# Kernel tuning notes

Hardware: AMD Instinct MI355X
Metric: run time of the kernel (lower is better)

## Reference

```python
import jax, jax.numpy as jnp
import numpy as np

N_NODES = 100000
N_EDGES = 640000
EMB = 128
BATCH = 16384
N_REL = 2
HIDDEN = [128, 64, 32]
LN_EPS = 1e-5
NORM_EPS = 1e-12


def setup_inputs() -> dict:
    key = jax.random.key(0)
    ks = jax.random.split(key, 24)
    inp = {}
    inp["user_indices"] = jax.random.randint(ks[0], (BATCH,), 0, N_NODES)
    inp["item_indices"] = jax.random.randint(ks[1], (BATCH,), 0, N_NODES)
    inp["edge_index"] = jax.random.randint(ks[2], (2, N_EDGES), 0, N_NODES)
    inp["edge_type"] = jax.random.randint(ks[3], (N_EDGES,), 0, N_REL)
    inp["edge_weight"] = jax.random.uniform(ks[4], (N_EDGES,), dtype=jnp.float32)
    # parameters
    s = 1.0 / np.sqrt(EMB)
    inp["embedding"] = jax.random.normal(ks[5], (N_NODES, EMB), jnp.float32) * 0.02
    inp["w1_rel"] = jax.random.normal(ks[6], (N_REL, EMB, EMB), jnp.float32) * s
    inp["w1_root"] = jax.random.normal(ks[7], (EMB, EMB), jnp.float32) * s
    inp["b1"] = jnp.zeros((EMB,), jnp.float32)
    inp["ln_g"] = jnp.ones((EMB,), jnp.float32)
    inp["ln_b"] = jnp.zeros((EMB,), jnp.float32)
    inp["w2_rel"] = jax.random.normal(ks[8], (N_REL, EMB, EMB), jnp.float32) * s
    inp["w2_root"] = jax.random.normal(ks[9], (EMB, EMB), jnp.float32) * s
    inp["b2"] = jnp.zeros((EMB,), jnp.float32)
    dims = [2 * EMB] + HIDDEN
    for i in range(len(HIDDEN)):
        inp[f"mlp_w{i}"] = jax.random.normal(ks[10 + i], (dims[i], dims[i + 1]), jnp.float32) / np.sqrt(dims[i])
        inp[f"mlp_b{i}"] = jnp.zeros((dims[i + 1],), jnp.float32)
    d_out = HIDDEN[-1] + EMB
    inp["out_w"] = jax.random.normal(ks[20], (d_out, 1), jnp.float32) / np.sqrt(d_out)
    inp["out_b"] = jnp.zeros((1,), jnp.float32)
    return inp


def rgcn_layer(x, edge_index, edge_type, edge_weight, w_rel, w_root, bias):
    # x: [N, D]; edge_index: [2, E]; per-relation linear on gathered source feats,
    # weighted scatter-add into destination nodes, plus root transform + bias.
    src, dst = edge_index[0], edge_index[1]
    x_j = x[src]  # [E, D] gather
    msg = jnp.zeros((x_j.shape[0], w_rel.shape[2]), x.dtype)
    for r in range(w_rel.shape[0]):  # small fixed relation count
        msg = msg + jnp.where((edge_type == r)[:, None], x_j @ w_rel[r], 0.0)
    msg = msg * edge_weight[:, None]
    agg = jax.ops.segment_sum(msg, dst, num_segments=x.shape[0])
    return agg + x @ w_root + bias


def layer_norm(x, g, b):
    mu = jnp.mean(x, axis=-1, keepdims=True)
    var = jnp.mean(jnp.square(x - mu), axis=-1, keepdims=True)
    return (x - mu) * jax.lax.rsqrt(var + LN_EPS) * g + b


def l2_normalize(x):
    n = jnp.sqrt(jnp.sum(jnp.square(x), axis=-1, keepdims=True))
    return x / jnp.maximum(n, NORM_EPS)


def reference(user_indices, item_indices, edge_index, edge_type, edge_weight,
              embedding, w1_rel, w1_root, b1, ln_g, ln_b, w2_rel, w2_root, b2,
              mlp_w0, mlp_b0, mlp_w1, mlp_b1, mlp_w2, mlp_b2, out_w, out_b):
    x = embedding  # embedding(arange(N)) == full table
    x = rgcn_layer(x, edge_index, edge_type, edge_weight, w1_rel, w1_root, b1)
    x = jax.nn.relu(x)
    # dropout is identity in eval mode
    x = layer_norm(x, ln_g, ln_b)
    x = rgcn_layer(x, edge_index, edge_type, edge_weight, w2_rel, w2_root, b2)

    u = x[user_indices]  # [B, D]
    v = x[item_indices]
    gmf = l2_normalize(u) * l2_normalize(v)  # [B, D]
    h = jnp.concatenate([u, v], axis=-1)  # [B, 2D]
    for w, b in ((mlp_w0, mlp_b0), (mlp_w1, mlp_b1), (mlp_w2, mlp_b2)):
        h = jax.nn.relu(h @ w + b)
    final = jnp.concatenate([gmf, h], axis=-1)  # [B, D + 32]
    score = jax.nn.sigmoid(final @ out_w + out_b)
    return jnp.squeeze(score, axis=-1)
```

## Files before the change

### kernel.cpp

```cpp
#include <hip/hip_runtime.h>
#include <cstddef>
#include <cstdint>

#define N_NODES 100000
#define N_EDGES 640000
#define EMBD    128
#define NBATCH  16384
#define CHUNK   1024
#define NCHUNK  ((N_NODES + CHUNK - 1) / CHUNK)

typedef short bf16x8 __attribute__((ext_vector_type(8)));
typedef float f32x4  __attribute__((ext_vector_type(4)));

__device__ __forceinline__ unsigned pack_split(float x) {
    unsigned u  = __float_as_uint(x);
    unsigned hi = (u + 0x7fffu + ((u >> 16) & 1u)) & 0xffff0000u;
    float    lo = x - __uint_as_float(hi);
    unsigned ul = __float_as_uint(lo);
    unsigned lw = ((ul + 0x7fffu + ((ul >> 16) & 1u)) >> 16) & 0xffffu;
    return hi | lw;
}
__device__ __forceinline__ float unpack_split(unsigned u) {
    return __uint_as_float(u & 0xffff0000u) + __uint_as_float(u << 16);
}

__global__ __launch_bounds__(256) void pack_kernel(
    const float* __restrict__ in, unsigned* __restrict__ out, int n)
{
    const int i = blockIdx.x * 256 + threadIdx.x;
    if (i < n) out[i] = pack_split(in[i]);
}

__global__ __launch_bounds__(256) void hist_kernel(
    const int* __restrict__ ei, int* __restrict__ cursor, int E)
{
    const int e = blockIdx.x * 256 + threadIdx.x;
    if (e < E) atomicAdd(&cursor[ei[E + e]], 1);
}

__global__ __launch_bounds__(256) void scan_local(
    int* __restrict__ cursor, int* __restrict__ bsum, int n)
{
    __shared__ int part[256];
    const int t    = threadIdx.x;
    const int base = blockIdx.x * CHUNK + t * 4;
    int v[4];
    int s = 0;
#pragma unroll
    for (int i = 0; i < 4; ++i) {
        const int idx = base + i;
        v[i] = (idx < n) ? cursor[idx] : 0;
        s += v[i];
    }
    part[t] = s;
    __syncthreads();
    for (int off = 1; off < 256; off <<= 1) {
        const int add = (t >= off) ? part[t - off] : 0;
        __syncthreads();
        part[t] += add;
        __syncthreads();
    }
    if (t == 255) bsum[blockIdx.x] = part[255];
    int run = (t == 0) ? 0 : part[t - 1];
#pragma unroll
    for (int i = 0; i < 4; ++i) {
        const int idx = base + i;
        if (idx < n) { cursor[idx] = run; run += v[i]; }
    }
}

__global__ __launch_bounds__(128) void scan_bsum(int* __restrict__ bsum)
{
    __shared__ int part[128];
    const int t = threadIdx.x;
    const int v = (t < NCHUNK) ? bsum[t] : 0;
    part[t] = v;
    __syncthreads();
    for (int off = 1; off < 128; off <<= 1) {
        const int add = (t >= off) ? part[t - off] : 0;
        __syncthreads();
        part[t] += add;
        __syncthreads();
    }
    if (t < NCHUNK) bsum[t] = part[t] - v;
}

__global__ __launch_bounds__(256) void scan_add(
    int* __restrict__ cursor, const int* __restrict__ bsum, int n)
{
    const int off  = bsum[blockIdx.x];
    const int base = blockIdx.x * CHUNK + threadIdx.x * 4;
#pragma unroll
    for (int i = 0; i < 4; ++i) {
        const int idx = base + i;
        if (idx < n) cursor[idx] += off;
    }
}

__global__ __launch_bounds__(256) void bucket_kernel(
    const int* __restrict__ ei, const int* __restrict__ et,
    const float* __restrict__ ew, int* __restrict__ cursor,
    int2* __restrict__ srec, int E)
{
    const int e = blockIdx.x * 256 + threadIdx.x;
    if (e >= E) return;
    const int src = ei[e];
    const int dst = ei[E + e];
    const int r   = et[e];
    const int pos = atomicAdd(&cursor[dst], 1);
    srec[pos] = make_int2(src | (r << 17), __float_as_int(ew[e]));
}

__global__ __launch_bounds__(256) void accum_csr(
    const unsigned* __restrict__ xp, const int2* __restrict__ srec,
    const int* __restrict__ cursor, unsigned* __restrict__ Ap, int N)
{
    const int wid  = blockIdx.x * 4 + (threadIdx.x >> 6);
    const int lane = threadIdx.x & 63;
    const int s = (wid == 0) ? 0 : cursor[wid - 1];
    const int e = cursor[wid];

    float ax = 0.f, ay = 0.f, bx = 0.f, by = 0.f;
    int i = s;
    for (; i + 3 < e; i += 4) {
        const int2 r0 = srec[i];
        const int2 r1 = srec[i + 1];
        const int2 r2 = srec[i + 2];
        const int2 r3 = srec[i + 3];
        const uint2 g0 = ((const uint2*)(xp + (size_t)(r0.x & 0x1FFFF) * EMBD))[lane];
        const uint2 g1 = ((const uint2*)(xp + (size_t)(r1.x & 0x1FFFF) * EMBD))[lane];
        const uint2 g2 = ((const uint2*)(xp + (size_t)(r2.x & 0x1FFFF) * EMBD))[lane];
        const uint2 g3 = ((const uint2*)(xp + (size_t)(r3.x & 0x1FFFF) * EMBD))[lane];
        const float w0 = __int_as_float(r0.y);
        const float w1 = __int_as_float(r1.y);
        const float w2 = __int_as_float(r2.y);
        const float w3 = __int_as_float(r3.y);
        {
            const float vx = unpack_split(g0.x), vy = unpack_split(g0.y);
            if (r0.x & (1 << 17)) { bx += vx * w0; by += vy * w0; }
            else                  { ax += vx * w0; ay += vy * w0; }
        }
        {
            const float vx = unpack_split(g1.x), vy = unpack_split(g1.y);
            if (r1.x & (1 << 17)) { bx += vx * w1; by += vy * w1; }
            else                  { ax += vx * w1; ay += vy * w1; }
        }
        {
            const float vx = unpack_split(g2.x), vy = unpack_split(g2.y);
            if (r2.x & (1 << 17)) { bx += vx * w2; by += vy * w2; }
            else                  { ax += vx * w2; ay += vy * w2; }
        }
        {
            const float vx = unpack_split(g3.x), vy = unpack_split(g3.y);
            if (r3.x & (1 << 17)) { bx += vx * w3; by += vy * w3; }
            else                  { ax += vx * w3; ay += vy * w3; }
        }
    }
    for (; i < e; ++i) {
        const int2 r0 = srec[i];
        const uint2 g0 = ((const uint2*)(xp + (size_t)(r0.x & 0x1FFFF) * EMBD))[lane];
        const float w0 = __int_as_float(r0.y);
        const float vx = unpack_split(g0.x), vy = unpack_split(g0.y);
        if (r0.x & (1 << 17)) { bx += vx * w0; by += vy * w0; }
        else                  { ax += vx * w0; ay += vy * w0; }
    }
    ((uint2*)(Ap + (size_t)wid * EMBD))[lane]             = make_uint2(pack_split(ax), pack_split(ay));
    ((uint2*)(Ap + ((size_t)N + wid) * EMBD))[lane]       = make_uint2(pack_split(bx), pack_split(by));
}

__global__ __launch_bounds__(256) void gemm_mfma(
    const unsigned* __restrict__ S0, const unsigned* __restrict__ S1,
    const unsigned* __restrict__ S2,
    const float* __restrict__ wrel, const float* __restrict__ wroot,
    const float* __restrict__ bias, const float* __restrict__ lng,
    const float* __restrict__ lnb, void* __restrict__ outv,
    int M, int do_ln)
{
    __shared__ unsigned short AsH[128 * 40], AsL[128 * 40];
    __shared__ unsigned short BsH[128 * 40], BsL[128 * 40];
    __shared__ float lnbuf[2][128][2];

    const int t    = threadIdx.x;
    const int wave = t >> 6;
    const int lane = t & 63;
    const int q    = lane >> 4;
    const int n    = lane & 15;
    const int wrow = wave & 1;
    const int wcol = wave >> 1;
    const int m0   = blockIdx.x * 128;

    const int arow  = t >> 1;
    const int ahalf = t & 1;
    const int bcol  = t & 127;
    const int bkh   = t >> 7;

    f32x4 acc[4][4];
#pragma unroll
    for (int rt = 0; rt < 4; ++rt)
#pragma unroll
        for (int ct = 0; ct < 4; ++ct)
            acc[rt][ct] = (f32x4){0.f, 0.f, 0.f, 0.f};

    for (int kc = 0; kc < 12; ++kc) {
        const unsigned* Sp  = (kc < 4) ? S0 : (kc < 8) ? S1 : S2;
        const int koff      = (kc & 3) * 32;
        const float* Wsrc   = (kc < 8) ? (wrel + (size_t)kc * 32 * EMBD)
                                       : (wroot + (size_t)(kc - 8) * 32 * EMBD);

        __syncthreads();

        {
            const int rg = m0 + arow;
            uint4 u[4];
            if (rg < M) {
                const unsigned* p = Sp + (size_t)rg * EMBD + koff + ahalf * 16;
                u[0] = *(const uint4*)(p);
                u[1] = *(const uint4*)(p + 4);
                u[2] = *(const uint4*)(p + 8);
                u[3] = *(const uint4*)(p + 12);
            } else {
                u[0] = u[1] = u[2] = u[3] = make_uint4(0u, 0u, 0u, 0u);
            }
            unsigned* dh = (unsigned*)AsH + arow * 20 + ahalf * 8;
            unsigned* dl = (unsigned*)AsL + arow * 20 + ahalf * 8;
            const unsigned* uu = (const unsigned*)u;
#pragma unroll
            for (int i = 0; i < 8; ++i) {
                const unsigned e0 = uu[2 * i], e1 = uu[2 * i + 1];
                dh[i] = (e1 & 0xffff0000u) | (e0 >> 16);
                dl[i] = (e1 << 16) | (e0 & 0xffffu);
            }
        }
        {
            unsigned p[16];
#pragma unroll
            for (int j = 0; j < 16; ++j)
                p[j] = pack_split(Wsrc[(size_t)(bkh * 16 + j) * EMBD + bcol]);
            unsigned* dh = (unsigned*)BsH + bcol * 20 + bkh * 8;
            unsigned* dl = (unsigned*)BsL + bcol * 20 + bkh * 8;
#pragma unroll
            for (int i = 0; i < 8; ++i) {
                const unsigned e0 = p[2 * i], e1 = p[2 * i + 1];
                dh[i] = (e1 & 0xffff0000u) | (e0 >> 16);
                dl[i] = (e1 << 16) | (e0 & 0xffffu);
            }
        }
        __syncthreads();

        bf16x8 ah[4], al[4], bh[4], bl[4];
#pragma unroll
        for (int rt = 0; rt < 4; ++rt) {
            const int r = wrow * 64 + rt * 16 + n;
            ah[rt] = *(const bf16x8*)&AsH[r * 40 + q * 8];
            al[rt] = *(const bf16x8*)&AsL[r * 40 + q * 8];
        }
#pragma unroll
        for (int ct = 0; ct < 4; ++ct) {
            const int c = wcol * 64 + ct * 16 + n;
            bh[ct] = *(const bf16x8*)&BsH[c * 40 + q * 8];
            bl[ct] = *(const bf16x8*)&BsL[c * 40 + q * 8];
        }
#pragma unroll
        for (int rt = 0; rt < 4; ++rt)
#pragma unroll
            for (int ct = 0; ct < 4; ++ct) {
                acc[rt][ct] = __builtin_amdgcn_mfma_f32_16x16x32_bf16(ah[rt], bh[ct], acc[rt][ct], 0, 0, 0);
                acc[rt][ct] = __builtin_amdgcn_mfma_f32_16x16x32_bf16(ah[rt], bl[ct], acc[rt][ct], 0, 0, 0);
                acc[rt][ct] = __builtin_amdgcn_mfma_f32_16x16x32_bf16(al[rt], bh[ct], acc[rt][ct], 0, 0, 0);
            }
    }

    float bb[4], gg[4], tb[4];
#pragma unroll
    for (int ct = 0; ct < 4; ++ct) {
        const int c = wcol * 64 + ct * 16 + n;
        bb[ct] = bias[c];
        gg[ct] = do_ln ? lng[c] : 0.f;
        tb[ct] = do_ln ? lnb[c] : 0.f;
    }

    if (do_ln) {
#pragma unroll
        for (int rt = 0; rt < 4; ++rt)
#pragma unroll
            for (int r = 0; r < 4; ++r) {
                float s = 0.f, sq = 0.f;
#pragma unroll
                for (int ct = 0; ct < 4; ++ct) {
                    float v = acc[rt][ct][r] + bb[ct];
                    v = fmaxf(v, 0.f);
                    acc[rt][ct][r] = v;
                    s += v; sq += v * v;
                }
#pragma unroll
                for (int off = 1; off < 16; off <<= 1) {
                    s  += __shfl_xor(s,  off, 64);
                    sq += __shfl_xor(sq, off, 64);
                }
                if (n == 0) {
                    const int row = wrow * 64 + rt * 16 + q * 4 + r;
                    lnbuf[wcol][row][0] = s;
                    lnbuf[wcol][row][1] = sq;
                }
            }
        __syncthreads();
        unsigned* outp = (unsigned*)outv;
#pragma unroll
        for (int rt = 0; rt < 4; ++rt)
#pragma unroll
            for (int r = 0; r < 4; ++r) {
                const int row = wrow * 64 + rt * 16 + q * 4 + r;
                const int rg  = m0 + row;
                const float s    = lnbuf[0][row][0] + lnbuf[1][row][0];
                const float sq   = lnbuf[0][row][1] + lnbuf[1][row][1];
                const float mu   = s * (1.0f / 128.0f);
                const float var  = sq * (1.0f / 128.0f) - mu * mu;
                const float rstd = rsqrtf(var + 1e-5f);
                if (rg < M) {
#pragma unroll
                    for (int ct = 0; ct < 4; ++ct) {
                        const int c = wcol * 64 + ct * 16 + n;
                        const float v = (acc[rt][ct][r] - mu) * rstd * gg[ct] + tb[ct];
                        outp[(size_t)rg * EMBD + c] = pack_split(v);
                    }
                }
            }
    } else {
        float* outp = (float*)outv;
#pragma unroll
        for (int rt = 0; rt < 4; ++rt)
#pragma unroll
            for (int r = 0; r < 4; ++r) {
                const int rg = m0 + wrow * 64 + rt * 16 + q * 4 + r;
                if (rg < M) {
#pragma unroll
                    for (int ct = 0; ct < 4; ++ct) {
                        const int c = wcol * 64 + ct * 16 + n;
                        outp[(size_t)rg * EMBD + c] = acc[rt][ct][r] + bb[ct];
                    }
                }
            }
    }
}

__global__ __launch_bounds__(256) void head_kernel(
    const float* __restrict__ x2, const int* __restrict__ ui, const int* __restrict__ vi,
    const float* __restrict__ mw0, const float* __restrict__ mb0,
    const float* __restrict__ mw1, const float* __restrict__ mb1,
    const float* __restrict__ mw2, const float* __restrict__ mb2,
    const float* __restrict__ ow, const float* __restrict__ ob,
    float* __restrict__ out, int B)
{
    __shared__ float h0[16][256];
    __shared__ float h1[16][128];
    __shared__ float h2[16][64];
    __shared__ float h3[16][32];
    __shared__ float ps_u[16][16], ps_v[16][16];
    __shared__ float inv_nunv[16];
    __shared__ float pg[16][16], ph[16][16];

    const int t   = threadIdx.x;
    const int bb0 = blockIdx.x * 16;

    for (int r = 0; r < 16; ++r) {
        const int b   = bb0 + r;
        const int idx = (t < 128) ? ui[b] : vi[b];
        const int c   = t & 127;
        h0[r][t] = x2[(size_t)idx * EMBD + c];
    }
    __syncthreads();

    {
        const int row = t >> 4, sub = t & 15;
        float su = 0.f, sv = 0.f;
#pragma unroll
        for (int k = 0; k < 8; ++k) {
            const float a = h0[row][sub + 16 * k];       su += a * a;
            const float b = h0[row][128 + sub + 16 * k]; sv += b * b;
        }
        ps_u[row][sub] = su; ps_v[row][sub] = sv;
    }
    __syncthreads();
    if (t < 16) {
        float su = 0.f, sv = 0.f;
#pragma unroll
        for (int k = 0; k < 16; ++k) { su += ps_u[t][k]; sv += ps_v[t][k]; }
        const float nu = fmaxf(sqrtf(su), 1e-12f);
        const float nv = fmaxf(sqrtf(sv), 1e-12f);
        inv_nunv[t] = 1.0f / (nu * nv);
    }
    __syncthreads();

    {
        const int c = t & 127, rr = t >> 7;
        float acc[8];
#pragma unroll
        for (int j = 0; j < 8; ++j) acc[j] = 0.f;
        for (int i = 0; i < 256; i += 4) {
            const float w0 = mw0[(i + 0) * 128 + c];
            const float w1 = mw0[(i + 1) * 128 + c];
            const float w2 = mw0[(i + 2) * 128 + c];
            const float w3 = mw0[(i + 3) * 128 + c];
#pragma unroll
            for (int j = 0; j < 8; ++j) {
                const float4 a = *(const float4*)&h0[rr * 8 + j][i];
                acc[j] += a.x * w0 + a.y * w1 + a.z * w2 + a.w * w3;
            }
        }
        const float bv = mb0[c];
#pragma unroll
        for (int j = 0; j < 8; ++j) h1[rr * 8 + j][c] = fmaxf(acc[j] + bv, 0.f);
    }
    __syncthreads();

    {
        const int c = t & 63, g = t >> 6;
        float acc[4] = {0.f, 0.f, 0.f, 0.f};
        for (int i = 0; i < 128; i += 4) {
            const float w0 = mw1[(i + 0) * 64 + c];
            const float w1 = mw1[(i + 1) * 64 + c];
            const float w2 = mw1[(i + 2) * 64 + c];
            const float w3 = mw1[(i + 3) * 64 + c];
#pragma unroll
            for (int j = 0; j < 4; ++j) {
                const float4 a = *(const float4*)&h1[g * 4 + j][i];
                acc[j] += a.x * w0 + a.y * w1 + a.z * w2 + a.w * w3;
            }
        }
        const float bv = mb1[c];
#pragma unroll
        for (int j = 0; j < 4; ++j) h2[g * 4 + j][c] = fmaxf(acc[j] + bv, 0.f);
    }
    __syncthreads();

    {
        const int c = t & 31, g = t >> 5;
        float acc[2] = {0.f, 0.f};
        for (int i = 0; i < 64; i += 4) {
            const float w0 = mw2[(i + 0) * 32 + c];
            const float w1 = mw2[(i + 1) * 32 + c];
            const float w2 = mw2[(i + 2) * 32 + c];
            const float w3 = mw2[(i + 3) * 32 + c];
#pragma unroll
            for (int j = 0; j < 2; ++j) {
                const float4 a = *(const float4*)&h2[g * 2 + j][i];
                acc[j] += a.x * w0 + a.y * w1 + a.z * w2 + a.w * w3;
            }
        }
        const float bv = mb2[c];
#pragma unroll
        for (int j = 0; j < 2; ++j) h3[g * 2 + j][c] = fmaxf(acc[j] + bv, 0.f);
    }
    __syncthreads();

    {
        const int row = t >> 4, sub = t & 15;
        float pgv = 0.f;
#pragma unroll
        for (int k = 0; k < 8; ++k) {
            const int c = sub + 16 * k;
            pgv += h0[row][c] * h0[row][128 + c] * ow[c];
        }
        const float phv = h3[row][sub]      * ow[128 + sub]
                        + h3[row][sub + 16] * ow[144 + sub];
        pg[row][sub] = pgv; ph[row][sub] = phv;
    }
    __syncthreads();
    if (t < 16) {
        float sg = 0.f, sh = 0.f;
#pragma unroll
        for (int k = 0; k < 16; ++k) { sg += pg[t][k]; sh += ph[t][k]; }
        const float z = sg * inv_nunv[t] + sh + ob[0];
        out[bb0 + t] = 1.0f / (1.0f + expf(-z));
    }
}

extern "C" void kernel_launch(void* const* d_in, const int* in_sizes, int n_in,
                              void* d_out, int out_size, void* d_ws, size_t ws_size,
                              hipStream_t stream)
{
    const int*   ui      = (const int*)d_in[0];
    const int*   vi      = (const int*)d_in[1];
    const int*   ei      = (const int*)d_in[2];
    const int*   et      = (const int*)d_in[3];
    const float* ew      = (const float*)d_in[4];
    const float* emb     = (const float*)d_in[5];
    const float* w1_rel  = (const float*)d_in[6];
    const float* w1_root = (const float*)d_in[7];
    const float* b1      = (const float*)d_in[8];
    const float* ln_g    = (const float*)d_in[9];
    const float* ln_b    = (const float*)d_in[10];
    const float* w2_rel  = (const float*)d_in[11];
    const float* w2_root = (const float*)d_in[12];
    const float* b2      = (const float*)d_in[13];
    const float* mw0     = (const float*)d_in[14];
    const float* mb0     = (const float*)d_in[15];
    const float* mw1     = (const float*)d_in[16];
    const float* mb1     = (const float*)d_in[17];
    const float* mw2     = (const float*)d_in[18];
    const float* mb2     = (const float*)d_in[19];
    const float* ow      = (const float*)d_in[20];
    const float* ob      = (const float*)d_in[21];
    float* out = (float*)d_out;

    const int N = N_NODES, E = N_EDGES, B = NBATCH;

    unsigned* Ap    = (unsigned*)d_ws;
    unsigned* xslot = Ap + (size_t)2 * N * EMBD;
    int2*     srec   = (int2*)(xslot + (size_t)N * EMBD);
    int*      cursor = (int*)(srec + E);
    int*      bsum   = cursor + N;

    float* x2 = (float*)Ap;

    pack_kernel<<<(N * EMBD + 255) / 256, 256, 0, stream>>>(emb, xslot, N * EMBD);

    hipMemsetAsync(cursor, 0, N * sizeof(int), stream);
    hist_kernel<<<(E + 255) / 256, 256, 0, stream>>>(ei, cursor, E);
    scan_local<<<NCHUNK, 256, 0, stream>>>(cursor, bsum, N);
    scan_bsum<<<1, 128, 0, stream>>>(bsum);
    scan_add<<<NCHUNK, 256, 0, stream>>>(cursor, bsum, N);
    bucket_kernel<<<(E + 255) / 256, 256, 0, stream>>>(ei, et, ew, cursor, srec, E);

    accum_csr<<<N / 4, 256, 0, stream>>>(xslot, srec, cursor, Ap, N);
    gemm_mfma<<<(N + 127) / 128, 256, 0, stream>>>(
        Ap, Ap + (size_t)N * EMBD, xslot,
        w1_rel, w1_root, b1, ln_g, ln_b,
        (void*)xslot , N, 1);

    accum_csr<<<N / 4, 256, 0, stream>>>(xslot, srec, cursor, Ap, N);
    gemm_mfma<<<(N + 127) / 128, 256, 0, stream>>>(
        Ap, Ap + (size_t)N * EMBD, xslot,
        w2_rel, w2_root, b2, nullptr, nullptr,
        (void*)x2 , N, 0);

    head_kernel<<<B / 16, 256, 0, stream>>>(
        x2, ui, vi, mw0, mb0, mw1, mb1, mw2, mb2, ow, ob, out, B);
}
```

Baseline: 501.2 us.

## Pre-pack GEMM weights once and register-prefetch the next K chunk

A new kernel converts both layers' relation and root weights once into transposed bf16 hi/lo planes. Each GEMM block now loads those planes with vector loads instead of re-splitting strided fp32 weights for every tile. The GEMM main loop prefetches the next K chunk into registers while MFMAs run on the current chunk, writes LDS with vector stores and adds a 3-block occupancy hint. The embedding pack and edge histogram kernels are fused into one launch. The fallback path for a small workspace indexes a packing array past its 8 entries, and the extra live prefetch registers may limit occupancy.

Result: slower. 535.4 us (+6.8%).

```diff
diff --git a/kernel.cpp b/kernel.cpp
--- a/kernel.cpp
+++ b/kernel.cpp
@@ -24,18 +24,38 @@
     return __uint_as_float(u & 0xffff0000u) + __uint_as_float(u << 16);
 }
 
-__global__ __launch_bounds__(256) void pack_kernel(
-    const float* __restrict__ in, unsigned* __restrict__ out, int n)
+__global__ __launch_bounds__(256) void pack_hist(
+    const float* __restrict__ emb, unsigned* __restrict__ xslot,
+    const int* __restrict__ ei, int* __restrict__ cursor, int n, int E)
 {
     const int i = blockIdx.x * 256 + threadIdx.x;
-    if (i < n) out[i] = pack_split(in[i]);
-}
-
-__global__ __launch_bounds__(256) void hist_kernel(
-    const int* __restrict__ ei, int* __restrict__ cursor, int E)
-{
-    const int e = blockIdx.x * 256 + threadIdx.x;
-    if (e < E) atomicAdd(&cursor[ei[E + e]], 1);
+    if (i < n) xslot[i] = pack_split(emb[i]);
+    if (i < E) atomicAdd(&cursor[ei[E + i]], 1);
+}
+
+__global__ void wpack_kernel(
+    const float* __restrict__ w1_rel, const float* __restrict__ w1_root,
+    const float* __restrict__ w2_rel, const float* __restrict__ w2_root,
+    unsigned short* __restrict__ WtH1, unsigned short* __restrict__ WtL1,
+    unsigned short* __restrict__ WtH2, unsigned short* __restrict__ WtL2)
+{
+    const int col = blockIdx.x;
+    const int k   = threadIdx.x;
+    const size_t o = (size_t)col * 384 + k;
+    {
+        const float x = (k < 256) ? w1_rel[(size_t)k * EMBD + col]
+                                  : w1_root[(size_t)(k - 256) * EMBD + col];
+        const unsigned p = pack_split(x);
+        WtH1[o] = (unsigned short)(p >> 16);
+        WtL1[o] = (unsigned short)(p & 0xffffu);
+    }
+    {
+        const float x = (k < 256) ? w2_rel[(size_t)k * EMBD + col]
+                                  : w2_root[(size_t)(k - 256) * EMBD + col];
+        const unsigned p = pack_split(x);
+        WtH2[o] = (unsigned short)(p >> 16);
+        WtL2[o] = (unsigned short)(p & 0xffffu);
+    }
 }
 
 __global__ __launch_bounds__(256) void scan_local(
@@ -164,13 +184,14 @@
         if (r0.x & (1 << 17)) { bx += vx * w0; by += vy * w0; }
         else                  { ax += vx * w0; ay += vy * w0; }
     }
-    ((uint2*)(Ap + (size_t)wid * EMBD))[lane]             = make_uint2(pack_split(ax), pack_split(ay));
-    ((uint2*)(Ap + ((size_t)N + wid) * EMBD))[lane]       = make_uint2(pack_split(bx), pack_split(by));
-}
-
-__global__ __launch_bounds__(256) void gemm_mfma(
+    ((uint2*)(Ap + (size_t)wid * EMBD))[lane]       = make_uint2(pack_split(ax), pack_split(ay));
+    ((uint2*)(Ap + ((size_t)N + wid) * EMBD))[lane] = make_uint2(pack_split(bx), pack_split(by));
+}
+
+__global__ __launch_bounds__(256, 3) void gemm_mfma(
     const unsigned* __restrict__ S0, const unsigned* __restrict__ S1,
     const unsigned* __restrict__ S2,
+    const unsigned short* __restrict__ WtH, const unsigned short* __restrict__ WtL,
     const float* __restrict__ wrel, const float* __restrict__ wroot,
     const float* __restrict__ bias, const float* __restrict__ lng,
     const float* __restrict__ lnb, void* __restrict__ outv,
@@ -189,10 +210,10 @@
     const int wcol = wave >> 1;
     const int m0   = blockIdx.x * 128;
 
-    const int arow  = t >> 1;
-    const int ahalf = t & 1;
-    const int bcol  = t & 127;
-    const int bkh   = t >> 7;
+    const int arow   = t >> 1;
+    const int ahalf  = t & 1;
+    const int bcol   = t & 127;
+    const int bplane = t >> 7;
 
     f32x4 acc[4][4];
 #pragma unroll
@@ -201,53 +222,77 @@
         for (int ct = 0; ct < 4; ++ct)
             acc[rt][ct] = (f32x4){0.f, 0.f, 0.f, 0.f};
 
+    uint4 au[4];
+    uint4 bw[4];
+
+    auto loadA = [&](int kc) {
+        const unsigned* Sp = (kc < 4) ? S0 : (kc < 8) ? S1 : S2;
+        const int rg = m0 + arow;
+        if (rg < M) {
+            const unsigned* p = Sp + (size_t)rg * EMBD + (kc & 3) * 32 + ahalf * 16;
+            au[0] = *(const uint4*)(p);
+            au[1] = *(const uint4*)(p + 4);
+            au[2] = *(const uint4*)(p + 8);
+            au[3] = *(const uint4*)(p + 12);
+        } else {
+            au[0] = au[1] = au[2] = au[3] = make_uint4(0u, 0u, 0u, 0u);
+        }
+    };
+    auto loadB = [&](int kc) {
+        if (WtH != nullptr) {
+            const unsigned short* W = bplane ? WtL : WtH;
+            const uint4* p = (const uint4*)(W + (size_t)bcol * 384 + kc * 32);
+            bw[0] = p[0]; bw[1] = p[1]; bw[2] = p[2]; bw[3] = p[3];
+        } else {
+            unsigned d[8];
+#pragma unroll
+            for (int i = 0; i < 8; ++i) d[i] = 0u;
+#pragma unroll
+            for (int j = 0; j < 32; ++j) {
+                const int kv = kc * 32 + j;
+                const float x = (kv < 256) ? wrel[(size_t)kv * EMBD + bcol]
+                                           : wroot[(size_t)(kv - 256) * EMBD + bcol];
+                const unsigned p = pack_split(x);
+                const unsigned part = bplane ? (p & 0xffffu) : (p >> 16);
+                d[j >> 1] |= part << (16 * (j & 1));
+            }
+            bw[0] = make_uint4(d[0], d[1], d[2], d[3]);
+            bw[1] = make_uint4(d[4], d[5], d[6], d[7]);
+            bw[2] = bw[3] = make_uint4(0u, 0u, 0u, 0u);
+        }
+    };
+    auto writeLDS = [&]() {
+        const unsigned* uu = (const unsigned*)au;
+        unsigned dh[8], dl[8];
+#pragma unroll
+        for (int i = 0; i < 8; ++i) {
+            const unsigned e0 = uu[2 * i], e1 = uu[2 * i + 1];
+            dh[i] = (e1 & 0xffff0000u) | (e0 >> 16);
+            dl[i] = (e1 << 16) | (e0 & 0xffffu);
+        }
+        uint4* pH = (uint4*)(AsH + arow * 40 + ahalf * 16);
+        uint4* pL = (uint4*)(AsL + arow * 40 + ahalf * 16);
+        pH[0] = make_uint4(dh[0], dh[1], dh[2], dh[3]);
+        pH[1] = make_uint4(dh[4], dh[5], dh[6], dh[7]);
+        pL[0] = make_uint4(dl[0], dl[1], dl[2], dl[3]);
+        pL[1] = make_uint4(dl[4], dl[5], dl[6], dl[7]);
+        if (WtH != nullptr) {
+            uint4* pB = (uint4*)((bplane ? BsL : BsH) + bcol * 40);
+            pB[0] = bw[0]; pB[1] = bw[1]; pB[2] = bw[2]; pB[3] = bw[3];
+        } else {
+            uint4* pB = (uint4*)((bplane ? BsL : BsH) + bcol * 40);
+            pB[0] = bw[0]; pB[1] = bw[1];
+        }
+    };
+
+    loadA(0); loadB(0);
+
     for (int kc = 0; kc < 12; ++kc) {
-        const unsigned* Sp  = (kc < 4) ? S0 : (kc < 8) ? S1 : S2;
-        const int koff      = (kc & 3) * 32;
-        const float* Wsrc   = (kc < 8) ? (wrel + (size_t)kc * 32 * EMBD)
-                                       : (wroot + (size_t)(kc - 8) * 32 * EMBD);
-
-        __syncthreads();
-
-        {
-            const int rg = m0 + arow;
-            uint4 u[4];
-            if (rg < M) {
-                const unsigned* p = Sp + (size_t)rg * EMBD + koff + ahalf * 16;
-                u[0] = *(const uint4*)(p);
-                u[1] = *(const uint4*)(p + 4);
-                u[2] = *(const uint4*)(p + 8);
-                u[3] = *(const uint4*)(p + 12);
-            } else {
-                u[0] = u[1] = u[2] = u[3] = make_uint4(0u, 0u, 0u, 0u);
-            }
-            unsigned* dh = (unsigned*)AsH + arow * 20 + ahalf * 8;
-            unsigned* dl = (unsigned*)AsL + arow * 20 + ahalf * 8;
-            const unsigned* uu = (const unsigned*)u;
-#pragma unroll
-            for (int i = 0; i < 8; ++i) {
-                const unsigned e0 = uu[2 * i], e1 = uu[2 * i + 1];
-                dh[i] = (e1 & 0xffff0000u) | (e0 >> 16);
-                dl[i] = (e1 << 16) | (e0 & 0xffffu);
-            }
-        }
-        {
-            unsigned p[16];
-#pragma unroll
-            for (int j = 0; j < 16; ++j)
-                p[j] = pack_split(Wsrc[(size_t)(bkh * 16 + j) * EMBD + bcol]);
-            unsigned* dh = (unsigned*)BsH + bcol * 20 + bkh * 8;
-            unsigned* dl = (unsigned*)BsL + bcol * 20 + bkh * 8;
-#pragma unroll
-            for (int i = 0; i < 8; ++i) {
-                const unsigned e0 = p[2 * i], e1 = p[2 * i + 1];
-                dh[i] = (e1 & 0xffff0000u) | (e0 >> 16);
-                dl[i] = (e1 << 16) | (e0 & 0xffffu);
-            }
-        }
-        __syncthreads();
-
-        bf16x8 ah[4], al[4], bh[4], bl[4];
+        writeLDS();
+        __syncthreads();
+        if (kc < 11) { loadA(kc + 1); loadB(kc + 1); }
+
+        bf16x8 ah[4], al[4];
 #pragma unroll
         for (int rt = 0; rt < 4; ++rt) {
             const int r = wrow * 64 + rt * 16 + n;
@@ -257,17 +302,16 @@
 #pragma unroll
         for (int ct = 0; ct < 4; ++ct) {
             const int c = wcol * 64 + ct * 16 + n;
-            bh[ct] = *(const bf16x8*)&BsH[c * 40 + q * 8];
-            bl[ct] = *(const bf16x8*)&BsL[c * 40 + q * 8];
-        }
-#pragma unroll
-        for (int rt = 0; rt < 4; ++rt)
-#pragma unroll
-            for (int ct = 0; ct < 4; ++ct) {
-                acc[rt][ct] = __builtin_amdgcn_mfma_f32_16x16x32_bf16(ah[rt], bh[ct], acc[rt][ct], 0, 0, 0);
-                acc[rt][ct] = __builtin_amdgcn_mfma_f32_16x16x32_bf16(ah[rt], bl[ct], acc[rt][ct], 0, 0, 0);
-                acc[rt][ct] = __builtin_amdgcn_mfma_f32_16x16x32_bf16(al[rt], bh[ct], acc[rt][ct], 0, 0, 0);
-            }
+            const bf16x8 bh = *(const bf16x8*)&BsH[c * 40 + q * 8];
+            const bf16x8 bl = *(const bf16x8*)&BsL[c * 40 + q * 8];
+#pragma unroll
+            for (int rt = 0; rt < 4; ++rt) {
+                acc[rt][ct] = __builtin_amdgcn_mfma_f32_16x16x32_bf16(ah[rt], bh, acc[rt][ct], 0, 0, 0);
+                acc[rt][ct] = __builtin_amdgcn_mfma_f32_16x16x32_bf16(ah[rt], bl, acc[rt][ct], 0, 0, 0);
+                acc[rt][ct] = __builtin_amdgcn_mfma_f32_16x16x32_bf16(al[rt], bh, acc[rt][ct], 0, 0, 0);
+            }
+        }
+        __syncthreads();
     }
 
     float bb[4], gg[4], tb[4];
@@ -511,12 +555,23 @@
     int*      cursor = (int*)(srec + E);
     int*      bsum   = cursor + N;
 
+    char* wt0 = (char*)(bsum + NCHUNK);
+    wt0 = (char*)(((uintptr_t)wt0 + 63) & ~(uintptr_t)63);
+    unsigned short* WtH1 = (unsigned short*)wt0;
+    unsigned short* WtL1 = WtH1 + 128 * 384;
+    unsigned short* WtH2 = WtL1 + 128 * 384;
+    unsigned short* WtL2 = WtH2 + 128 * 384;
+    const size_t need_wt = (size_t)((char*)(WtL2 + 128 * 384) - (char*)d_ws);
+    const bool have_wt = (ws_size >= need_wt);
+
     float* x2 = (float*)Ap;
 
-    pack_kernel<<<(N * EMBD + 255) / 256, 256, 0, stream>>>(emb, xslot, N * EMBD);
-
     hipMemsetAsync(cursor, 0, N * sizeof(int), stream);
-    hist_kernel<<<(E + 255) / 256, 256, 0, stream>>>(ei, cursor, E);
+    pack_hist<<<(N * EMBD + 255) / 256, 256, 0, stream>>>(emb, xslot, ei, cursor, N * EMBD, E);
+    if (have_wt)
+        wpack_kernel<<<128, 384, 0, stream>>>(w1_rel, w1_root, w2_rel, w2_root,
+                                              WtH1, WtL1, WtH2, WtL2);
+
     scan_local<<<NCHUNK, 256, 0, stream>>>(cursor, bsum, N);
     scan_bsum<<<1, 128, 0, stream>>>(bsum);
     scan_add<<<NCHUNK, 256, 0, stream>>>(cursor, bsum, N);
@@ -525,12 +580,14 @@
     accum_csr<<<N / 4, 256, 0, stream>>>(xslot, srec, cursor, Ap, N);
     gemm_mfma<<<(N + 127) / 128, 256, 0, stream>>>(
         Ap, Ap + (size_t)N * EMBD, xslot,
+        have_wt ? WtH1 : nullptr, have_wt ? WtL1 : nullptr,
         w1_rel, w1_root, b1, ln_g, ln_b,
         (void*)xslot , N, 1);
 
     accum_csr<<<N / 4, 256, 0, stream>>>(xslot, srec, cursor, Ap, N);
     gemm_mfma<<<(N + 127) / 128, 256, 0, stream>>>(
         Ap, Ap + (size_t)N * EMBD, xslot,
+        have_wt ? WtH2 : nullptr, have_wt ? WtL2 : nullptr,
         w2_rel, w2_root, b2, nullptr, nullptr,
         (void*)x2 , N, 0);
 
```
